# Optimization experiments

Hardware: AMD Instinct MI355X
Metric: run time of the kernel (lower is better)

## Reference

```python
import jax, jax.numpy as jnp
import numpy as np

B, N, C, H = 2, 2048, 1024, 16
D = C // H  # head dim 64


def setup_inputs() -> dict:
    key = jax.random.key(0)
    k1, k2, k3, k4 = jax.random.split(key, 4)
    x = jax.random.normal(k1, (B, N, C), dtype=jnp.float32)
    s = 1.0 / np.sqrt(C)
    Wq = jax.random.normal(k2, (C, C), dtype=jnp.float32) * s    # [out,in] torch layout
    Wkv = jax.random.normal(k3, (2 * C, C), dtype=jnp.float32) * s
    Wo = jax.random.normal(k4, (C, C), dtype=jnp.float32) * s
    bo = jnp.zeros((C,), dtype=jnp.float32)
    return {"x": x, "Wq": Wq, "Wkv": Wkv, "Wo": Wo, "bo": bo}


def reference(x, Wq, Wkv, Wo, bo):
    # projections (torch Linear: y = x @ W.T)
    q = x @ Wq.T                      # [B,N,C]
    kv = x @ Wkv.T                    # [B,N,2C] (context = x)
    k, v = jnp.split(kv, 2, axis=-1)  # each [B,N,C]

    def heads(t):  # [B,N,C] -> [B,H,N,D]
        return t.reshape(B, N, H, D).transpose(0, 2, 1, 3)

    q, k, v = heads(q), heads(k), heads(v)
    # elu+1 feature map
    q = jax.nn.elu(q) + 1.0
    k = jax.nn.elu(k) + 1.0
    # quadratic kernelized attention, as in the source
    sim = jnp.einsum('bhqd,bhkd->bhqk', q, k)               # [B,H,N,N]
    Z = 1.0 / (jnp.einsum('bhqd,bhd->bhq', q, k.sum(axis=2)) + 1e-6)
    out = jnp.einsum('bhqk,bhkd->bhqd', sim * Z[..., None], v)  # [B,H,N,D]
    out = out.transpose(0, 2, 1, 3).reshape(B, N, C)
    return out @ Wo.T + bo
```

## Files before the change

### kernel.cpp

```cpp
#include <hip/hip_runtime.h>
#include <math.h>

#define C_DIM 1024
#define B_SZ 2
#define N_SEQ 2048
#define M_ROWS (B_SZ * N_SEQ)
#define KDIM 1024
#define G1_SLOT 10240
#define G2_SLOT 6144

typedef float  f32x4   __attribute__((ext_vector_type(4)));
typedef short  bf16x8  __attribute__((ext_vector_type(8)));
typedef short  short4v __attribute__((ext_vector_type(4)));
typedef short  short8v __attribute__((ext_vector_type(8)));

__device__ __forceinline__ float elu1(float v) {
    return v > 0.f ? v + 1.f : expf(v);
}

__device__ __forceinline__ ushort f2bf(float f) {
    union { float f; unsigned u; } x; x.f = f;
    unsigned r = (x.u + 0x7fffu + ((x.u >> 16) & 1u)) >> 16;
    return (ushort)r;
}
__device__ __forceinline__ float bf2f(ushort b) {
    union { unsigned u; float f; } x; x.u = ((unsigned)b) << 16;
    return x.f;
}

#define VMCNT(n) asm volatile("s_waitcnt vmcnt(" #n ")" ::: "memory")
#define LGKMBAR do {                                                  \
        asm volatile("s_waitcnt lgkmcnt(0)" ::: "memory");            \
        __builtin_amdgcn_sched_barrier(0);                            \
        __builtin_amdgcn_s_barrier();                                 \
    } while (0)

__device__ __forceinline__ void gl16(const ushort* g, ushort* l) {
    __builtin_amdgcn_global_load_lds(
        (const __attribute__((address_space(1))) unsigned int*)g,
        (__attribute__((address_space(3))) unsigned int*)l,
        16, 0, 0);
}

__global__ __launch_bounds__(256)
void split_all_kernel(const float* __restrict__ x, const float* __restrict__ Wq,
                      const float* __restrict__ Wkv, const float* __restrict__ Wo,
                      ushort* __restrict__ xhi, ushort* __restrict__ Whi,
                      ushort* __restrict__ Wohi)
{
    const int i = blockIdx.x * 256 + threadIdx.x;
    const float* src; ushort* dh; int off;
    if (i < 524288)        { src = x;   dh = xhi;  off = i; }
    else if (i < 655360)   { src = Wq;  dh = Whi;  off = i - 524288; }
    else if (i < 917504)   { src = Wkv; dh = Whi + (1u << 20); off = i - 655360; }
    else                   { src = Wo;  dh = Wohi; off = i - 917504; }

    const float4 a = ((const float4*)src)[off * 2];
    const float4 b = ((const float4*)src)[off * 2 + 1];
    const float v[8] = {a.x, a.y, a.z, a.w, b.x, b.y, b.z, b.w};
    ushort hv[8];
    #pragma unroll
    for (int j = 0; j < 8; ++j) hv[j] = f2bf(v[j]);
    short8v H = {(short)hv[0],(short)hv[1],(short)hv[2],(short)hv[3],
                 (short)hv[4],(short)hv[5],(short)hv[6],(short)hv[7]};
    *(short8v*)&dh[(size_t)off * 8] = H;
}

__global__ __launch_bounds__(256, 2)
void gemm1_kernel(const ushort* __restrict__ Ahi, const ushort* __restrict__ Bhi,
                  ushort* __restrict__ dst)
{
    extern __shared__ ushort smem[];

    const int bid = blockIdx.x;
    const int wg  = (bid & 7) * 64 + (bid >> 3);
    const int m0  = (wg >> 4) * 128;
    const int n0  = (wg & 15) * 192;

    const int t    = threadIdx.x;
    const int lane = t & 63;
    const int w    = t >> 6;
    const int wr   = w >> 1;
    const int wc   = w & 1;

    const int gch     = (t & 3) ^ ((t >> 3) & 3);
    const size_t rowA  = (size_t)(m0 + (t >> 2)) * KDIM + gch * 8;
    const size_t rowA2 = rowA + (size_t)64 * KDIM;
    const size_t rowB  = (size_t)(n0 + (t >> 2)) * KDIM + gch * 8;
    const size_t rowB2 = rowB + (size_t)64 * KDIM;
    const size_t rowB3 = rowB + (size_t)128 * KDIM;
    const int wl      = w * 512;

    const int frow = lane & 15;
    const int cc   = (lane >> 4) ^ ((lane >> 1) & 3);
    const int aoff = (wr * 64 + frow) * 32 + cc * 8;
    const int boff = 4096 + (wc * 96 + frow) * 32 + cc * 8;

    f32x4 acc[4][6];
    #pragma unroll
    for (int mi = 0; mi < 4; ++mi)
        #pragma unroll
        for (int nj = 0; nj < 6; ++nj)
            acc[mi][nj] = (f32x4){0.f, 0.f, 0.f, 0.f};

    #define STAGE1(slotp, koff)                                              \
        do {                                                                 \
            ushort* sl_ = (slotp);                                           \
            gl16(Ahi + rowA  + (koff), sl_ + wl);                            \
            gl16(Ahi + rowA2 + (koff), sl_ + 2048 + wl);                     \
            gl16(Bhi + rowB  + (koff), sl_ + 4096 + wl);                     \
            gl16(Bhi + rowB2 + (koff), sl_ + 6144 + wl);                     \
            gl16(Bhi + rowB3 + (koff), sl_ + 8192 + wl);                     \
        } while (0)

    STAGE1(smem, 0);
    STAGE1(smem + G1_SLOT, 32);
    STAGE1(smem + 2 * G1_SLOT, 64);

    #pragma unroll 1
    for (int kt = 0; kt < 32; ++kt) {
        ushort* sh = smem + (kt & 3) * G1_SLOT;

        if (kt <= 29) { VMCNT(10); } else if (kt == 30) { VMCNT(5); } else { VMCNT(0); }
        LGKMBAR;
        if (kt <= 28) STAGE1(smem + ((kt + 3) & 3) * G1_SLOT, (kt + 3) * 32);

        bf16x8 ah[4], bh[6];
        #pragma unroll
        for (int mi = 0; mi < 4; ++mi)
            ah[mi] = *(const bf16x8*)(sh + aoff + mi * 512);
        #pragma unroll
        for (int nj = 0; nj < 6; ++nj)
            bh[nj] = *(const bf16x8*)(sh + boff + nj * 512);
        __builtin_amdgcn_s_setprio(1);
        #pragma unroll
        for (int mi = 0; mi < 4; ++mi)
            #pragma unroll
            for (int nj = 0; nj < 6; ++nj)
                acc[mi][nj] = __builtin_amdgcn_mfma_f32_16x16x32_bf16(
                    ah[mi], bh[nj], acc[mi][nj], 0, 0, 0);
        __builtin_amdgcn_s_setprio(0);
    }
    #undef STAGE1

    const int erow  = m0 + wr * 64 + (lane >> 4) * 4;
    const int ecol0 = n0 + wc * 96 + frow;
    #pragma unroll
    for (int mi = 0; mi < 4; ++mi) {
        #pragma unroll
        for (int j = 0; j < 4; ++j) {
            const int row = erow + mi * 16 + j;
            #pragma unroll
            for (int nj = 0; nj < 6; ++nj) {
                const int col = ecol0 + nj * 16;
                float v = acc[mi][nj][j];
                if (col < 2048) v = elu1(v);
                dst[(size_t)row * 3072 + col] = f2bf(v);
            }
        }
    }
}

__global__ __launch_bounds__(256, 2)
void gemm2_kernel(const ushort* __restrict__ O1, const ushort* __restrict__ Wo,
                  const float* __restrict__ bias, float* __restrict__ dst)
{
    __shared__ ushort smem[4 * G2_SLOT];

    const int bid = blockIdx.x;
    const int wg  = (bid & 7) * 64 + (bid >> 3);
    const int m0  = (wg >> 3) * 64;
    const int n0  = (wg & 7) * 128;

    const int t    = threadIdx.x;
    const int lane = t & 63;
    const int w    = t >> 6;

    const int gch     = (t & 3) ^ ((t >> 3) & 3);
    const size_t rowA  = (size_t)(m0 + (t >> 2)) * KDIM + gch * 8;
    const size_t rowB  = (size_t)(n0 + (t >> 2)) * KDIM + gch * 8;
    const size_t rowB2 = rowB + (size_t)64 * KDIM;
    const int wl      = w * 512;

    const int frow = lane & 15;
    const int cc   = (lane >> 4) ^ ((lane >> 1) & 3);
    const int aoff = frow * 32 + cc * 8;
    const int boff = 2048 + (w * 32 + frow) * 32 + cc * 8;

    f32x4 acc[4][2];
    #pragma unroll
    for (int mi = 0; mi < 4; ++mi)
        #pragma unroll
        for (int nj = 0; nj < 2; ++nj)
            acc[mi][nj] = (f32x4){0.f, 0.f, 0.f, 0.f};

    #define STAGE2(slotp, koff)                                              \
        do {                                                                 \
            ushort* p_ = (slotp);                                            \
            gl16(O1 + rowA  + (koff), p_ + wl);                              \
            gl16(Wo + rowB  + (koff), p_ + 2048 + wl);                       \
            gl16(Wo + rowB2 + (koff), p_ + 4096 + wl);                       \
        } while (0)

    STAGE2(smem, 0);
    STAGE2(smem + G2_SLOT, 32);
    STAGE2(smem + 2 * G2_SLOT, 64);

    #pragma unroll 1
    for (int kt = 0; kt < 32; ++kt) {
        ushort* sh = smem + (kt & 3) * G2_SLOT;

        if (kt <= 29) { VMCNT(6); } else if (kt == 30) { VMCNT(3); } else { VMCNT(0); }
        LGKMBAR;
        if (kt <= 28) STAGE2(smem + ((kt + 3) & 3) * G2_SLOT, (kt + 3) * 32);

        bf16x8 ah[4], bh[2];
        #pragma unroll
        for (int mi = 0; mi < 4; ++mi)
            ah[mi] = *(const bf16x8*)(sh + aoff + mi * 512);
        #pragma unroll
        for (int nj = 0; nj < 2; ++nj)
            bh[nj] = *(const bf16x8*)(sh + boff + nj * 512);
        __builtin_amdgcn_s_setprio(1);
        #pragma unroll
        for (int mi = 0; mi < 4; ++mi)
            #pragma unroll
            for (int nj = 0; nj < 2; ++nj)
                acc[mi][nj] = __builtin_amdgcn_mfma_f32_16x16x32_bf16(
                    ah[mi], bh[nj], acc[mi][nj], 0, 0, 0);
        __builtin_amdgcn_s_setprio(0);
    }
    #undef STAGE2

    const int erow  = m0 + (lane >> 4) * 4;
    const int ecol0 = n0 + w * 32 + frow;
    #pragma unroll
    for (int mi = 0; mi < 4; ++mi) {
        #pragma unroll
        for (int j = 0; j < 4; ++j) {
            const int row = erow + mi * 16 + j;
            #pragma unroll
            for (int nj = 0; nj < 2; ++nj) {
                const int col = ecol0 + nj * 16;
                dst[(size_t)row * 1024 + col] = acc[mi][nj][j] + bias[col];
            }
        }
    }
}

__global__ __launch_bounds__(256)
void kv_partial_kernel(const ushort* __restrict__ QKV, float* __restrict__ KVp)
{
    const int bh = blockIdx.x;
    const int s  = blockIdx.y;
    const int b  = bh >> 4;
    const int h  = bh & 15;
    const int t  = threadIdx.x;

    __shared__ float ks[16][64];
    __shared__ float vs[16][64];
    __shared__ float red[4160];

    const int srow = t >> 4;
    const int scol = (t & 15) * 4;
    const size_t gk = (size_t)(b * N_SEQ + s * 256) * 3072 + 1024 + h * 64 + scol;
    const size_t gv = gk + 1024;

    const int rs = t >> 6;
    const int dg = (t >> 3) & 7;
    const int eg = t & 7;
    const int d0 = dg * 8;
    const int e0 = eg * 8;

    float acc[8][8];
    #pragma unroll
    for (int i = 0; i < 8; ++i)
        #pragma unroll
        for (int j = 0; j < 8; ++j) acc[i][j] = 0.f;
    float aks[8] = {0.f, 0.f, 0.f, 0.f, 0.f, 0.f, 0.f, 0.f};

    short4v kr = *(const short4v*)&QKV[gk + (size_t)srow * 3072];
    short4v vr = *(const short4v*)&QKV[gv + (size_t)srow * 3072];

    for (int it = 0; it < 16; ++it) {
        __syncthreads();
        ks[srow][scol + 0] = bf2f((ushort)kr[0]);
        ks[srow][scol + 1] = bf2f((ushort)kr[1]);
        ks[srow][scol + 2] = bf2f((ushort)kr[2]);
        ks[srow][scol + 3] = bf2f((ushort)kr[3]);
        vs[srow][scol + 0] = bf2f((ushort)vr[0]);
        vs[srow][scol + 1] = bf2f((ushort)vr[1]);
        vs[srow][scol + 2] = bf2f((ushort)vr[2]);
        vs[srow][scol + 3] = bf2f((ushort)vr[3]);
        __syncthreads();
        if (it < 15) {
            kr = *(const short4v*)&QKV[gk + (size_t)((it + 1) * 16 + srow) * 3072];
            vr = *(const short4v*)&QKV[gv + (size_t)((it + 1) * 16 + srow) * 3072];
        }
        #pragma unroll
        for (int rr = 0; rr < 4; ++rr) {
            const int r = rs * 4 + rr;
            const float4 ka = *(const float4*)&ks[r][d0];
            const float4 kb = *(const float4*)&ks[r][d0 + 4];
            const float4 va = *(const float4*)&vs[r][e0];
            const float4 vb = *(const float4*)&vs[r][e0 + 4];
            const float k8[8] = {ka.x, ka.y, ka.z, ka.w, kb.x, kb.y, kb.z, kb.w};
            const float v8[8] = {va.x, va.y, va.z, va.w, vb.x, vb.y, vb.z, vb.w};
            #pragma unroll
            for (int i = 0; i < 8; ++i)
                #pragma unroll
                for (int j = 0; j < 8; ++j)
                    acc[i][j] += k8[i] * v8[j];
            if (eg == 0) {
                #pragma unroll
                for (int i = 0; i < 8; ++i) aks[i] += k8[i];
            }
        }
    }

    #pragma unroll 1
    for (int step = 1; step < 4; ++step) {
        __syncthreads();
        if (rs == step) {
            #pragma unroll
            for (int i = 0; i < 8; ++i)
                #pragma unroll
                for (int j = 0; j < 8; ++j)
                    red[(d0 + i) * 64 + e0 + j] = acc[i][j];
            if (eg == 0) {
                #pragma unroll
                for (int i = 0; i < 8; ++i) red[4096 + d0 + i] = aks[i];
            }
        }
        __syncthreads();
        if (rs == 0) {
            #pragma unroll
            for (int i = 0; i < 8; ++i)
                #pragma unroll
                for (int j = 0; j < 8; ++j)
                    acc[i][j] += red[(d0 + i) * 64 + e0 + j];
            if (eg == 0) {
                #pragma unroll
                for (int i = 0; i < 8; ++i) aks[i] += red[4096 + d0 + i];
            }
        }
    }

    if (rs == 0) {
        float* outp = KVp + ((size_t)s * 32 + bh) * 4160;
        #pragma unroll
        for (int i = 0; i < 8; ++i) {
            float4 o0 = {acc[i][0], acc[i][1], acc[i][2], acc[i][3]};
            float4 o1 = {acc[i][4], acc[i][5], acc[i][6], acc[i][7]};
            *(float4*)(outp + (d0 + i) * 64 + e0)     = o0;
            *(float4*)(outp + (d0 + i) * 64 + e0 + 4) = o1;
        }
        if (eg == 0) {
            #pragma unroll
            for (int i = 0; i < 8; ++i) outp[4096 + d0 + i] = aks[i];
        }
    }
}

__global__ __launch_bounds__(256)
void kv_reduce_kernel(const float* __restrict__ KVp, float* __restrict__ KVf)
{
    const int idx = blockIdx.x * 256 + threadIdx.x;
    if (idx < 32 * 4160) {
        float s = 0.f;
        #pragma unroll
        for (int i = 0; i < 8; ++i) s += KVp[(size_t)i * (32 * 4160) + idx];
        KVf[idx] = s;
    }
}

__global__ __launch_bounds__(256)
void attn_apply_kernel(const ushort* __restrict__ QKV, const float* __restrict__ KVf,
                       ushort* __restrict__ O1)
{
    const int bh = blockIdx.x;
    const int b = bh >> 4, h = bh & 15;
    const int n0 = blockIdx.y * 16;
    const int t = threadIdx.x;
    const int r  = t >> 4;
    const int e0 = (t & 15) * 4;

    __shared__ float kvs[64][68];
    __shared__ float qs[16][68];
    __shared__ float ksums[64];

    const float* kvb = KVf + (size_t)bh * 4160;
    for (int i = t; i < 4096; i += 256)
        kvs[i >> 6][i & 63] = kvb[i];
    if (t < 64) ksums[t] = kvb[4096 + t];
    {
        const int rr = t >> 4, cc2 = (t & 15) * 4;
        short4v q4 = *(const short4v*)&QKV[(size_t)(b * N_SEQ + n0 + rr) * 3072 + h * 64 + cc2];
        qs[rr][cc2 + 0] = bf2f((ushort)q4[0]);
        qs[rr][cc2 + 1] = bf2f((ushort)q4[1]);
        qs[rr][cc2 + 2] = bf2f((ushort)q4[2]);
        qs[rr][cc2 + 3] = bf2f((ushort)q4[3]);
    }
    __syncthreads();

    float4 acc = {0.f, 0.f, 0.f, 0.f};
    float accz = 0.f;
    #pragma unroll
    for (int d = 0; d < 64; ++d) {
        const float qv = qs[r][d];
        const float4 kvv = *(const float4*)&kvs[d][e0];
        acc.x += qv * kvv.x; acc.y += qv * kvv.y;
        acc.z += qv * kvv.z; acc.w += qv * kvv.w;
        accz += qv * ksums[d];
    }
    const float Z = 1.f / (accz + 1e-6f);
    const size_t off = (size_t)(b * N_SEQ + n0 + r) * C_DIM + h * 64 + e0;
    short4v H = {(short)f2bf(acc.x * Z), (short)f2bf(acc.y * Z),
                 (short)f2bf(acc.z * Z), (short)f2bf(acc.w * Z)};
    *(short4v*)&O1[off] = H;
}

extern "C" void kernel_launch(void* const* d_in, const int* in_sizes, int n_in,
                              void* d_out, int out_size, void* d_ws, size_t ws_size,
                              hipStream_t stream)
{
    const float* x   = (const float*)d_in[0];
    const float* Wq  = (const float*)d_in[1];
    const float* Wkv = (const float*)d_in[2];
    const float* Wo  = (const float*)d_in[3];
    const float* bo  = (const float*)d_in[4];
    float* out = (float*)d_out;

    float* ws    = (float*)d_ws;
    ushort* QKVu = (ushort*)ws;
    float* KVp   = ws + (size_t)M_ROWS * 3072 / 2;
    float* KVf   = KVp + (size_t)8 * 32 * 4160;
    ushort* xhi  = (ushort*)(KVf + 32 * 4160);
    ushort* Whi  = xhi + (size_t)M_ROWS * 1024;
    ushort* Wohi = Whi + (size_t)3072 * 1024;
    ushort* O1   = xhi;

    hipFuncSetAttribute((const void*)gemm1_kernel,
                        hipFuncAttributeMaxDynamicSharedMemorySize, 81920);

    split_all_kernel<<<dim3(4096), 256, 0, stream>>>(
        x, Wq, Wkv, Wo, xhi, Whi, Wohi);

    gemm1_kernel<<<dim3(512), 256, 81920, stream>>>(xhi, Whi, QKVu);

    kv_partial_kernel<<<dim3(32, 8), 256, 0, stream>>>(QKVu, KVp);
    kv_reduce_kernel<<<dim3((32 * 4160 + 255) / 256), 256, 0, stream>>>(KVp, KVf);

    attn_apply_kernel<<<dim3(32, 128), 256, 0, stream>>>(QKVu, KVf, O1);

    gemm2_kernel<<<dim3(512), 256, 0, stream>>>(O1, Wohi, bo, out);
}
```

Before: 99.66 us.

## Fuse KV reduction into partial kernel via last-block atomic counter; remap GEMM1 tiles

Removes the separate kv_reduce launch. Each (batch, head) group of 8 split blocks increments an atomic counter, and the last block to finish sums the partials into KVf. The counters are zeroed in the split kernel. GEMM1's block-to-tile mapping is also changed so that each XCD-strided group of blocks covers a compact 8x8 tile region, aiming for better L2 reuse. The fused path depends on threadfence ordering and adds a serial reduction tail in the last block of each group.

```diff
diff --git a/kernel.cpp b/kernel.cpp
--- a/kernel.cpp
+++ b/kernel.cpp
@@ -46,9 +46,10 @@
 void split_all_kernel(const float* __restrict__ x, const float* __restrict__ Wq,
                       const float* __restrict__ Wkv, const float* __restrict__ Wo,
                       ushort* __restrict__ xhi, ushort* __restrict__ Whi,
-                      ushort* __restrict__ Wohi)
+                      ushort* __restrict__ Wohi, int* __restrict__ counters)
 {
     const int i = blockIdx.x * 256 + threadIdx.x;
+    if (i < 32) counters[i] = 0;
     const float* src; ushort* dh; int off;
     if (i < 524288)        { src = x;   dh = xhi;  off = i; }
     else if (i < 655360)   { src = Wq;  dh = Whi;  off = i - 524288; }
@@ -73,9 +74,10 @@
     extern __shared__ ushort smem[];
 
     const int bid = blockIdx.x;
-    const int wg  = (bid & 7) * 64 + (bid >> 3);
-    const int m0  = (wg >> 4) * 128;
-    const int n0  = (wg & 15) * 192;
+    const int r   = bid & 7;
+    const int ii  = bid >> 3;
+    const int m0  = ((r >> 1) * 8 + (ii >> 3)) * 128;
+    const int n0  = ((r & 1) * 8 + (ii & 7)) * 192;
 
     const int t    = threadIdx.x;
     const int lane = t & 63;
@@ -249,7 +251,8 @@
 }
 
 __global__ __launch_bounds__(256)
-void kv_partial_kernel(const ushort* __restrict__ QKV, float* __restrict__ KVp)
+void kv_partial_kernel(const ushort* __restrict__ QKV, float* __restrict__ KVp,
+                       float* __restrict__ KVf, int* __restrict__ counters)
 {
     const int bh = blockIdx.x;
     const int s  = blockIdx.y;
@@ -260,6 +263,7 @@
     __shared__ float ks[16][64];
     __shared__ float vs[16][64];
     __shared__ float red[4160];
+    __shared__ int last_flag;
 
     const int srow = t >> 4;
     const int scol = (t & 15) * 4;
@@ -360,17 +364,20 @@
             for (int i = 0; i < 8; ++i) outp[4096 + d0 + i] = aks[i];
         }
     }
-}
-
-__global__ __launch_bounds__(256)
-void kv_reduce_kernel(const float* __restrict__ KVp, float* __restrict__ KVf)
-{
-    const int idx = blockIdx.x * 256 + threadIdx.x;
-    if (idx < 32 * 4160) {
-        float s = 0.f;
-        #pragma unroll
-        for (int i = 0; i < 8; ++i) s += KVp[(size_t)i * (32 * 4160) + idx];
-        KVf[idx] = s;
+
+    __threadfence();
+    __syncthreads();
+    if (t == 0) last_flag = atomicAdd(&counters[bh], 1);
+    __syncthreads();
+    if (last_flag == 7) {
+        __threadfence();
+        for (int idx = t; idx < 4160; idx += 256) {
+            float sum = 0.f;
+            #pragma unroll
+            for (int p = 0; p < 8; ++p)
+                sum += KVp[((size_t)p * 32 + bh) * 4160 + idx];
+            KVf[(size_t)bh * 4160 + idx] = sum;
+        }
     }
 }
 
@@ -435,7 +442,8 @@
     ushort* QKVu = (ushort*)ws;
     float* KVp   = ws + (size_t)M_ROWS * 3072 / 2;
     float* KVf   = KVp + (size_t)8 * 32 * 4160;
-    ushort* xhi  = (ushort*)(KVf + 32 * 4160);
+    int*   ctrs  = (int*)(KVf + 32 * 4160);
+    ushort* xhi  = (ushort*)(ctrs + 64);
     ushort* Whi  = xhi + (size_t)M_ROWS * 1024;
     ushort* Wohi = Whi + (size_t)3072 * 1024;
     ushort* O1   = xhi;
@@ -444,12 +452,11 @@
                         hipFuncAttributeMaxDynamicSharedMemorySize, 81920);
 
     split_all_kernel<<<dim3(4096), 256, 0, stream>>>(
-        x, Wq, Wkv, Wo, xhi, Whi, Wohi);
+        x, Wq, Wkv, Wo, xhi, Whi, Wohi, ctrs);
 
     gemm1_kernel<<<dim3(512), 256, 81920, stream>>>(xhi, Whi, QKVu);
 
-    kv_partial_kernel<<<dim3(32, 8), 256, 0, stream>>>(QKVu, KVp);
-    kv_reduce_kernel<<<dim3((32 * 4160 + 255) / 256), 256, 0, stream>>>(KVp, KVf);
+    kv_partial_kernel<<<dim3(32, 8), 256, 0, stream>>>(QKVu, KVp, KVf, ctrs);
 
     attn_apply_kernel<<<dim3(32, 128), 256, 0, stream>>>(QKVu, KVf, O1);
 
```

After: 128.8 us. +29.2%, slower.
